# Kernel optimization log

Measured on AMD Instinct MI355X. Metric: run time of the kernel, lower is better.

## Reference

```python
import math
import jax, jax.numpy as jnp
import numpy as np

Q = 0.15
B, T, D = 32, 2048, 512
NEG = -1e9


def setup_inputs() -> dict:
    key = jax.random.key(0)
    k1, k2 = jax.random.split(key)
    H = jax.random.normal(k1, (B, T, D), dtype=jnp.float32)
    lengths = jax.random.randint(k2, (B,), 1, T + 1, dtype=jnp.int32)
    return {"H": H, "lengths": lengths}


def reference(H, lengths):
    Bc, Tc, Dc = H.shape
    kmax = int(math.ceil(Tc * Q))  # static upper bound on per-row k

    # per-timestep L2 norm, masked beyond each row's length
    valid = jnp.arange(Tc)[None, :] < lengths[:, None]            # [B,T]
    scores = jnp.where(valid, jnp.linalg.norm(H, axis=2), NEG)    # [B,T]

    # per-row k = clamp(ceil(len*q), 1)
    k_vals = jnp.maximum(
        jnp.ceil(lengths.astype(jnp.float32) * Q).astype(jnp.int32), 1
    )                                                              # [B]

    # take a static top-kmax, then mask down to each row's dynamic k
    _, top_idx = jax.lax.top_k(scores, kmax)                      # [B,kmax]
    gathered = jnp.take_along_axis(H, top_idx[:, :, None], axis=1)  # [B,kmax,D]
    sel = (jnp.arange(kmax)[None, :] < k_vals[:, None]).astype(H.dtype)  # [B,kmax]

    pooled = jnp.einsum("bkd,bk->bd", gathered, sel) / k_vals[:, None].astype(H.dtype)
    return pooled
```

## Files before the change

### kernel.cpp

```cpp
#include <hip/hip_runtime.h>
#include <stdint.h>

static constexpr int BB = 32;
static constexpr int TT = 2048;
static constexpr int DD = 512;
static constexpr int IDX_STRIDE = 320;

__global__ __launch_bounds__(256) void topq_norms(
    const float* __restrict__ H, const int* __restrict__ lengths,
    unsigned int* __restrict__ keys)
{
    const int wave = threadIdx.x >> 6;
    const int lane = threadIdx.x & 63;
    const int row  = (blockIdx.x << 2) + wave;
    const float4* p = reinterpret_cast<const float4*>(H) + (size_t)row * (DD / 4);
    float4 a = p[lane];
    float4 c = p[lane + 64];
    float s = a.x*a.x + a.y*a.y + a.z*a.z + a.w*a.w
            + c.x*c.x + c.y*c.y + c.z*c.z + c.w*c.w;
    #pragma unroll
    for (int off = 32; off; off >>= 1) s += __shfl_xor(s, off);
    if (lane == 0) {
        const int b = row >> 11;
        const int t = row & (TT - 1);
        unsigned int key = 0u;
        if (t < lengths[b]) key = __float_as_uint(sqrtf(s)) + 1u;
        keys[row] = key;
    }
}

__global__ __launch_bounds__(256) void topq_select(
    const unsigned int* __restrict__ keys, const int* __restrict__ lengths,
    unsigned short* __restrict__ idx, int* __restrict__ karr,
    float* __restrict__ kf)
{
    __shared__ unsigned int sk[TT];
    __shared__ int sred[4];
    __shared__ int spos;
    const int b   = blockIdx.x;
    const int tid = threadIdx.x;
    for (int i = tid; i < TT; i += 256) sk[i] = keys[b * TT + i];
    if (tid == 0) spos = 0;
    __syncthreads();

    const int len = lengths[b];
    int k = (int)ceilf((float)len * 0.15f);
    if (k < 1) k = 1;

    unsigned long long lo = 0, hi = 1ull << 43;
    while (hi - lo > 1ull) {
        const unsigned long long mid = (lo + hi) >> 1;
        int cnt = 0;
        #pragma unroll
        for (int r = 0; r < TT / 256; ++r) {
            const int i = tid + r * 256;
            const unsigned long long ck =
                ((unsigned long long)sk[i] << 11) | (unsigned long long)(TT - 1 - i);
            cnt += (ck >= mid) ? 1 : 0;
        }
        #pragma unroll
        for (int off = 32; off; off >>= 1) cnt += __shfl_xor(cnt, off);
        if ((tid & 63) == 0) sred[tid >> 6] = cnt;
        __syncthreads();
        const int total = sred[0] + sred[1] + sred[2] + sred[3];
        __syncthreads();
        if (total >= k) lo = mid; else hi = mid;
    }

    const unsigned long long thr = lo;
    for (int i = tid; i < TT; i += 256) {
        const unsigned long long ck =
            ((unsigned long long)sk[i] << 11) | (unsigned long long)(TT - 1 - i);
        if (ck >= thr) {
            const int p = atomicAdd(&spos, 1);
            idx[b * IDX_STRIDE + p] = (unsigned short)i;
        }
    }
    if (tid == 0) { karr[b] = k; kf[b] = (float)k; }
}

__global__ __launch_bounds__(128) void topq_pool(
    const float* __restrict__ H, const unsigned short* __restrict__ idx,
    const int* __restrict__ karr, const float* __restrict__ kf,
    float* __restrict__ out)
{
    const int b = blockIdx.x;
    const int c = blockIdx.y * 128 + threadIdx.x;
    const int k = karr[b];
    const unsigned short* mi = idx + b * IDX_STRIDE;
    const float* Hb = H + (size_t)b * TT * DD;
    float a0 = 0.f, a1 = 0.f, a2 = 0.f, a3 = 0.f;
    int j = 0;
    for (; j + 4 <= k; j += 4) {
        const int t0 = mi[j], t1 = mi[j + 1], t2 = mi[j + 2], t3 = mi[j + 3];
        a0 += Hb[(size_t)t0 * DD + c];
        a1 += Hb[(size_t)t1 * DD + c];
        a2 += Hb[(size_t)t2 * DD + c];
        a3 += Hb[(size_t)t3 * DD + c];
    }
    for (; j < k; ++j) a0 += Hb[(size_t)mi[j] * DD + c];
    out[b * DD + c] = ((a0 + a1) + (a2 + a3)) / kf[b];
}

extern "C" void kernel_launch(void* const* d_in, const int* in_sizes, int n_in,
                              void* d_out, int out_size, void* d_ws, size_t ws_size,
                              hipStream_t stream)
{
    const float* H       = (const float*)d_in[0];
    const int*   lengths = (const int*)d_in[1];
    float*       out     = (float*)d_out;

    char* ws = (char*)d_ws;
    unsigned int*   keys = (unsigned int*)ws;
    unsigned short* idx  = (unsigned short*)(ws + (size_t)BB * TT * 4);
    int*   karr = (int*)  (ws + (size_t)BB * TT * 4 + BB * IDX_STRIDE * 2);
    float* kf   = (float*)(ws + (size_t)BB * TT * 4 + BB * IDX_STRIDE * 2 + BB * 4);

    topq_norms <<<dim3(BB * TT / 4), 256, 0, stream>>>(H, lengths, keys);
    topq_select<<<dim3(BB),          256, 0, stream>>>(keys, lengths, idx, karr, kf);
    topq_pool  <<<dim3(BB, 4),       128, 0, stream>>>(H, idx, karr, kf, out);
}
```

Before: 239.1 us.

## Fuse top-k selection and pooling into one kernel with single-wave radix search

Merges the selection and pooling kernels into one 512-thread block per batch row, keeping the selected index list in shared memory instead of global workspace, which removes one launch and the global round-trip. The threshold binary search now runs in a single wave with the keys held in registers, so each of the 43 iterations no longer needs two block barriers. The tradeoff is that the other 7 waves sit idle during the search, pooling uses only 32 blocks instead of 128, and each thread keeps 32 keys in registers.

```diff
diff --git a/kernel.cpp b/kernel.cpp
--- a/kernel.cpp
+++ b/kernel.cpp
@@ -4,7 +4,7 @@
 static constexpr int BB = 32;
 static constexpr int TT = 2048;
 static constexpr int DD = 512;
-static constexpr int IDX_STRIDE = 320;
+static constexpr int LMAX = 320;
 
 __global__ __launch_bounds__(256) void topq_norms(
     const float* __restrict__ H, const int* __restrict__ lengths,
@@ -29,77 +29,82 @@
     }
 }
 
-__global__ __launch_bounds__(256) void topq_select(
+__global__ __launch_bounds__(512) void topq_selpool(
     const unsigned int* __restrict__ keys, const int* __restrict__ lengths,
-    unsigned short* __restrict__ idx, int* __restrict__ karr,
-    float* __restrict__ kf)
+    const float* __restrict__ H, float* __restrict__ out)
 {
-    __shared__ unsigned int sk[TT];
-    __shared__ int sred[4];
-    __shared__ int spos;
+    __shared__ unsigned int   sk[TT];
+    __shared__ unsigned short slist[LMAX];
+    __shared__ int scount;
+    __shared__ int skk;
+
     const int b   = blockIdx.x;
     const int tid = threadIdx.x;
-    for (int i = tid; i < TT; i += 256) sk[i] = keys[b * TT + i];
-    if (tid == 0) spos = 0;
+    for (int i = tid; i < TT; i += 512) sk[i] = keys[b * TT + i];
+    if (tid == 0) scount = 0;
     __syncthreads();
 
-    const int len = lengths[b];
-    int k = (int)ceilf((float)len * 0.15f);
-    if (k < 1) k = 1;
+    if (tid < 64) {
+        const int lane = tid;
+        unsigned int kreg[32];
+        #pragma unroll
+        for (int j = 0; j < 32; ++j) kreg[j] = sk[j * 64 + lane];
 
-    unsigned long long lo = 0, hi = 1ull << 43;
-    while (hi - lo > 1ull) {
-        const unsigned long long mid = (lo + hi) >> 1;
-        int cnt = 0;
-        #pragma unroll
-        for (int r = 0; r < TT / 256; ++r) {
-            const int i = tid + r * 256;
-            const unsigned long long ck =
-                ((unsigned long long)sk[i] << 11) | (unsigned long long)(TT - 1 - i);
-            cnt += (ck >= mid) ? 1 : 0;
+        const int len = lengths[b];
+        int k = (int)ceilf((float)len * 0.15f);
+        if (k < 1) k = 1;
+
+        unsigned long long lo = 0, hi = 1ull << 43;
+        while (hi - lo > 1ull) {
+            const unsigned long long mid = (lo + hi) >> 1;
+            int cnt = 0;
+            #pragma unroll
+            for (int j = 0; j < 32; ++j) {
+                const unsigned long long ck =
+                    ((unsigned long long)kreg[j] << 11) |
+                    (unsigned long long)(TT - 1 - (j * 64 + lane));
+                cnt += (ck >= mid) ? 1 : 0;
+            }
+            #pragma unroll
+            for (int off = 32; off; off >>= 1) cnt += __shfl_xor(cnt, off);
+            if (cnt >= k) lo = mid; else hi = mid;
         }
         #pragma unroll
-        for (int off = 32; off; off >>= 1) cnt += __shfl_xor(cnt, off);
-        if ((tid & 63) == 0) sred[tid >> 6] = cnt;
-        __syncthreads();
-        const int total = sred[0] + sred[1] + sred[2] + sred[3];
-        __syncthreads();
-        if (total >= k) lo = mid; else hi = mid;
+        for (int j = 0; j < 32; ++j) {
+            const unsigned long long ck =
+                ((unsigned long long)kreg[j] << 11) |
+                (unsigned long long)(TT - 1 - (j * 64 + lane));
+            if (ck >= lo) {
+                const int p = atomicAdd(&scount, 1);
+                slist[p] = (unsigned short)(j * 64 + lane);
+            }
+        }
+        if (tid == 0) skk = k;
     }
+    __syncthreads();
 
-    const unsigned long long thr = lo;
-    for (int i = tid; i < TT; i += 256) {
-        const unsigned long long ck =
-            ((unsigned long long)sk[i] << 11) | (unsigned long long)(TT - 1 - i);
-        if (ck >= thr) {
-            const int p = atomicAdd(&spos, 1);
-            idx[b * IDX_STRIDE + p] = (unsigned short)i;
-        }
+    const int k = skk;
+    const float* Hb = H + (size_t)b * TT * DD;
+    float a0 = 0.f, a1 = 0.f, a2 = 0.f, a3 = 0.f,
+          a4 = 0.f, a5 = 0.f, a6 = 0.f, a7 = 0.f;
+    int j = 0;
+    for (; j + 8 <= k; j += 8) {
+        const int t0 = slist[j],     t1 = slist[j + 1],
+                  t2 = slist[j + 2], t3 = slist[j + 3],
+                  t4 = slist[j + 4], t5 = slist[j + 5],
+                  t6 = slist[j + 6], t7 = slist[j + 7];
+        a0 += Hb[(size_t)t0 * DD + tid];
+        a1 += Hb[(size_t)t1 * DD + tid];
+        a2 += Hb[(size_t)t2 * DD + tid];
+        a3 += Hb[(size_t)t3 * DD + tid];
+        a4 += Hb[(size_t)t4 * DD + tid];
+        a5 += Hb[(size_t)t5 * DD + tid];
+        a6 += Hb[(size_t)t6 * DD + tid];
+        a7 += Hb[(size_t)t7 * DD + tid];
     }
-    if (tid == 0) { karr[b] = k; kf[b] = (float)k; }
-}
-
-__global__ __launch_bounds__(128) void topq_pool(
-    const float* __restrict__ H, const unsigned short* __restrict__ idx,
-    const int* __restrict__ karr, const float* __restrict__ kf,
-    float* __restrict__ out)
-{
-    const int b = blockIdx.x;
-    const int c = blockIdx.y * 128 + threadIdx.x;
-    const int k = karr[b];
-    const unsigned short* mi = idx + b * IDX_STRIDE;
-    const float* Hb = H + (size_t)b * TT * DD;
-    float a0 = 0.f, a1 = 0.f, a2 = 0.f, a3 = 0.f;
-    int j = 0;
-    for (; j + 4 <= k; j += 4) {
-        const int t0 = mi[j], t1 = mi[j + 1], t2 = mi[j + 2], t3 = mi[j + 3];
-        a0 += Hb[(size_t)t0 * DD + c];
-        a1 += Hb[(size_t)t1 * DD + c];
-        a2 += Hb[(size_t)t2 * DD + c];
-        a3 += Hb[(size_t)t3 * DD + c];
-    }
-    for (; j < k; ++j) a0 += Hb[(size_t)mi[j] * DD + c];
-    out[b * DD + c] = ((a0 + a1) + (a2 + a3)) / kf[b];
+    for (; j < k; ++j) a0 += Hb[(size_t)slist[j] * DD + tid];
+    const float s = ((a0 + a1) + (a2 + a3)) + ((a4 + a5) + (a6 + a7));
+    out[b * DD + tid] = s / (float)k;
 }
 
 extern "C" void kernel_launch(void* const* d_in, const int* in_sizes, int n_in,
@@ -110,13 +115,8 @@
     const int*   lengths = (const int*)d_in[1];
     float*       out     = (float*)d_out;
 
-    char* ws = (char*)d_ws;
-    unsigned int*   keys = (unsigned int*)ws;
-    unsigned short* idx  = (unsigned short*)(ws + (size_t)BB * TT * 4);
-    int*   karr = (int*)  (ws + (size_t)BB * TT * 4 + BB * IDX_STRIDE * 2);
-    float* kf   = (float*)(ws + (size_t)BB * TT * 4 + BB * IDX_STRIDE * 2 + BB * 4);
+    unsigned int* keys = (unsigned int*)d_ws;
 
-    topq_norms <<<dim3(BB * TT / 4), 256, 0, stream>>>(H, lengths, keys);
-    topq_select<<<dim3(BB),          256, 0, stream>>>(keys, lengths, idx, karr, kf);
-    topq_pool  <<<dim3(BB, 4),       128, 0, stream>>>(H, idx, karr, kf, out);
+    topq_norms  <<<dim3(BB * TT / 4), 256, 0, stream>>>(H, lengths, keys);
+    topq_selpool<<<dim3(BB),          512, 0, stream>>>(keys, lengths, H, out);
 }
```

After: 215.6 us. -9.8%, faster.
